# Kernel tuning notes

Hardware: AMD Instinct MI355X
Metric: run time of the kernel (lower is better)

## Reference

```python
import jax, jax.numpy as jnp
import numpy as np

# ParamsJR('JR') defaults, all variances 0 -> fixed constants; w_bb and lm are the fit params.
DT = 1e-4                      # step_size
VMAX, V0, R = 5.0, 6.0, 0.56   # sigmoid params
U_UB = 500.0                   # u_2ndsys_ub
G_EFF = 0.01 + 1000.0          # lb + relu(g)
C1_EFF, C2_EFF = 0.01 + 135.0, 0.01 + 135.0 * 0.8
C3_EFF, C4_EFF = 0.01 + 135.0 * 0.25, 0.01 + 135.0 * 0.25
STD_EFF = 150.0 + 100.0        # noise_std_lb + relu(std_in)
K_EFF = 0.5 + 5.0              # k_lb + relu(k)
A_EFF, a_EFF = 3.25, 1.0 + 100.0   # 0+relu(A), 1+relu(a)
B_EFF, b_EFF = 22.0, 1.0 + 50.0    # 0+relu(B), 1+relu(b)
CY0, Y0, MU = 5.0, 2.0, 0.5
CONDUCT_LB = 1.5


def _sig(x):
    return VMAX / (1.0 + jnp.exp(R * (V0 - x)))


def _sys2nd(A, a, u, x, v):
    return A * a * u - 2.0 * a * v - a * a * x


def _sat(x):  # state saturation 1000*tanh(x/1000)
    return 1000.0 * jnp.tanh(x / 1000.0)


def setup_inputs() -> dict:
    N, H, B, OUT, BUF = 200, 20, 400, 64, 500
    key = jax.random.key(0)
    ks = jax.random.split(key, 7)
    return {
        "input": jax.random.normal(ks[0], (N, H, B), jnp.float32),
        "noise_in": jax.random.normal(ks[1], (N, H, B, 3), jnp.float32),
        "noise_out": jax.random.normal(ks[2], (N, B), jnp.float32),
        "hx": jax.random.uniform(ks[3], (N, 6), jnp.float32),
        "hE": jnp.zeros((N, BUF), jnp.float32),
        "w_bb": jnp.full((N, N), 0.05, jnp.float32),  # zeros + 0.05 init
        "lm": jax.random.normal(ks[4], (OUT, N), jnp.float32),
        "sc": jax.random.uniform(ks[5], (N, N), jnp.float32),
        "dist": jax.random.randint(ks[6], (N, N), 0, 100, dtype=jnp.int32),
    }


def _forward(input, noise_in, noise_out, hx, hE, w_bb, lm, sc, delays):
    OUT = lm.shape[0]
    # connectivity normalization (done once, outside the time loop, as in torch)
    w = jnp.exp(w_bb) * sc
    wl = jnp.log1p(0.5 * (w + w.T))
    w_n = wl / jnp.linalg.norm(wl)             # (N,N)
    dg = -jnp.diag(jnp.sum(w_n, axis=1))       # (N,N) Laplacian diagonal
    # lead-field normalization: rowwise L1 (torch: sqrt(lm**2).sum(1)), then column mean-center
    lm1 = lm / jnp.abs(lm).sum(axis=1, keepdims=True)
    lm_t = lm1 - lm1.sum(axis=0, keepdims=True) / OUT

    def inner(carry, xs):
        M, E, I, Mv, Ev, Iv, hEb = carry
        u, nE = xs                                              # (N,1) each
        Ed = jnp.take_along_axis(hEb, delays, axis=1)           # delayed M buffer
        LEd = jnp.sum(w_n * Ed.T, axis=1, keepdims=True)        # (N,1)
        rM = _sig(E - I)
        rE = STD_EFF * nE + G_EFF * (LEd + dg @ E) + C2_EFF * _sig(C1_EFF * M)
        rI = C4_EFF * _sig(C3_EFF * M)
        ddM = M + DT * Mv
        ddE = E + DT * Ev
        ddI = I + DT * Iv
        ddMv = Mv + DT * _sys2nd(A_EFF, a_EFF, U_UB * jnp.tanh(rM / U_UB), M, Mv)
        ddEv = Ev + DT * _sys2nd(A_EFF, a_EFF, K_EFF * u + U_UB * jnp.tanh(rE / U_UB), E, Ev)
        ddIv = Iv + DT * _sys2nd(B_EFF, b_EFF, U_UB * jnp.tanh(rI / U_UB), I, Iv)
        M, E, I = _sat(ddM), _sat(ddE), _sat(ddI)
        Mv, Ev, Iv = _sat(ddMv), _sat(ddEv), _sat(ddIv)
        hEb = hEb.at[:, 0].set(M[:, 0])
        return (M, E, I, Mv, Ev, Iv, hEb), None

    def outer(carry, xs):
        u_tr, n_tr = xs                                         # (H,N,1) each
        carry, _ = jax.lax.scan(inner, carry, (u_tr, n_tr))
        M, E, I, Mv, Ev, Iv, hEb = carry
        hEb = jnp.concatenate([M, hEb[:, :-1]], axis=1)         # shift delay buffer per TR
        eeg = CY0 * (lm_t @ (E - I)) - Y0                       # (OUT,1)
        return (M, E, I, Mv, Ev, Iv, hEb), eeg[:, 0]

    M, E, I = hx[:, 0:1], hx[:, 1:2], hx[:, 2:3]
    Mv, Ev, Iv = hx[:, 3:4], hx[:, 4:5], hx[:, 5:6]
    u_all = jnp.transpose(input, (2, 1, 0))[..., None]          # (B,H,N,1)
    nE_all = jnp.transpose(noise_in[..., 0], (2, 1, 0))[..., None]
    carry, eeg = jax.lax.scan(outer, (M, E, I, Mv, Ev, Iv, hE), (u_all, nE_all))
    M, E, I, Mv, Ev, Iv, _ = carry
    current_state = jnp.concatenate([M, E, I, Mv, Ev, Iv], axis=1)  # (N,6)
    return eeg.T, current_state                                 # eeg_batch (OUT,B)


def reference(input, noise_in, noise_out, hx, hE, w_bb, lm, sc, dist):
    delays = (dist.astype(jnp.float32) / (CONDUCT_LB + MU)).astype(jnp.int32)
    return _forward(input, noise_in, noise_out, hx, hE, w_bb, lm, sc, delays)
```

## Files before the change

### kernel.cpp

```cpp
#include <hip/hip_runtime.h>
#include <math.h>

namespace {

constexpr int N_   = 200;
constexpr int H_   = 20;
constexpr int B_   = 400;
constexpr int OUT_ = 64;
constexpr int BUF_ = 500;
constexpr int NT_  = 1024;
constexpr int HD_  = 50;
constexpr int HS_  = 51;
constexpr int GT0  = 224;
constexpr int NG_  = 800;
constexpr int EPT  = 50;
constexpr int CAP  = 16;
constexpr int UNR  = 12;
constexpr int RW_  = 256;
constexpr int NFREE = NT_ - RW_;
constexpr int SLAB  = H_ * N_;

constexpr float L2E = 1.4426950408889634f;
constexpr float LN2 = 0.6931471805599453f;

constexpr float DT_  = 0.0001f;
constexpr float G_   = 1000.01f;
constexpr float C1_  = 135.01f;
constexpr float C2_  = 108.01f;
constexpr float C3_  = 33.76f;
constexpr float C4_  = 33.76f;
constexpr float STD_ = 250.0f;
constexpr float K_   = 5.5f;
constexpr float CY0_ = 5.0f;
constexpr float Y0_  = 2.0f;

constexpr float RL2E = 0.56f * L2E;
constexpr float V0R  = 6.0f * RL2E;
constexpr float TU_  = 2.0f * L2E / 500.0f;
constexpr float TS_  = 2.0f * L2E / 1000.0f;

constexpr float KMv = 0.9798f, KMu = 0.0328250f, KMx = 1.0201f;
constexpr float KEv = 0.9798f, KEu = 0.0328250f, KEx = 1.0201f;
constexpr float KIv = 0.9898f, KIu = 0.1122000f, KIx = 0.2601f;

__device__ __forceinline__ float fexp2(float x){ return __builtin_amdgcn_exp2f(x); }
__device__ __forceinline__ float flog2(float x){ return __builtin_amdgcn_logf(x); }
__device__ __forceinline__ float frcp (float x){ return __builtin_amdgcn_rcpf(x); }

__device__ __forceinline__ float sigf(float x){
    return 5.0f * frcp(1.0f + fexp2(fmaf(-RL2E, x, V0R)));
}
__device__ __forceinline__ float tanh500(float x){
    return 500.0f - 1000.0f * frcp(1.0f + fexp2(x * TU_));
}
__device__ __forceinline__ float satf(float x){
    return 1000.0f - 2000.0f * frcp(1.0f + fexp2(x * TS_));
}
__device__ __forceinline__ float wl_f(const float* __restrict__ wbb,
                                      const float* __restrict__ sc,
                                      int i, int j){
    float w0 = fexp2(wbb[i*N_+j]*L2E) * sc[i*N_+j];
    float w1 = fexp2(wbb[j*N_+i]*L2E) * sc[j*N_+i];
    return flog2(1.0f + 0.5f*(w0+w1)) * LN2;
}

__global__ void __launch_bounds__(NT_)
jansen_kernel(
    const float* __restrict__ input,
    const float* __restrict__ noise_in,
    const float* __restrict__ hx,
    const float* __restrict__ hEin,
    const float* __restrict__ wbb,
    const float* __restrict__ lm,
    const float* __restrict__ sc,
    const int*   __restrict__ dist,
    float* __restrict__ out,
    float2* __restrict__ tab)
{
    __shared__ float histT[N_*HS_];
    __shared__ float uslab[H_*N_];
    __shared__ float neslab[H_*N_];
    __shared__ float d0w_l[CAP*N_];
    __shared__ unsigned char d0j_l[CAP*N_];
    __shared__ float d1w_l[CAP*N_];
    __shared__ unsigned char d1j_l[CAP*N_];
    __shared__ float led_part[4*N_];
    __shared__ float2 mpair[2*N_];
    __shared__ float emi[N_];
    __shared__ float colmean[N_];
    __shared__ float lmrs[OUT_];
    __shared__ float red_s[NT_/64];
    __shared__ float norm_s;
    __shared__ int   rbar;

    const int t = threadIdx.x;
    const bool isr = (t < N_);
    const bool isg = (t >= GT0);
    const int  gt  = t - GT0;
    const int  grow  = gt >> 2;
    const int  gslot = gt & 3;
    const int  jbase = gslot * EPT;
    const int  tb    = gt * EPT;

    int sidx[5];
    int goff[5];

    if (t == 0) rbar = 0;
    if (t < OUT_){
        float s2 = 0.f;
        for (int j=0;j<N_;++j) s2 += fabsf(lm[t*N_+j]);
        lmrs[t] = s2;
    }
    float M=0,E=0,I=0,Mv=0,Ev=0,Iv=0, rowsum=0, ledst=0, hE0v=0;
    int cnt0=0, cnt1=0;
    #pragma unroll
    for (int r=0;r<5;++r){ sidx[r]=0; goff[r]=0; }
    if (isg){
        #pragma unroll
        for (int r=0;r<5;++r){
            int p = r*NG_ + gt;
            int hh = p / N_, ii = p - hh*N_;
            sidx[r] = hh*N_ + ii;
            goff[r] = ii*(H_*B_) + hh*B_;
            uslab[sidx[r]]  = input[goff[r]];
            neslab[sidx[r]] = noise_in[goff[r]*3];
        }
    }
    if (isr){
        for (int k=1;k<HD_;++k) histT[t*HS_ + (HD_-k)] = hEin[t*BUF_+k];
        hE0v = hEin[t*BUF_];
        M=hx[t*6+0]; E=hx[t*6+1]; I=hx[t*6+2];
        Mv=hx[t*6+3]; Ev=hx[t*6+4]; Iv=hx[t*6+5];
    }
    __syncthreads();

    float ss = 0.f, rs = 0.f;
    for (int m=0;m<EPT;++m){
        float w = 0.f; int d = 2;
        int j = jbase + m;
        if (isg){
            d = dist[j*N_+grow] >> 1;
            w = wl_f(wbb, sc, grow, j);
        }
        ss = fmaf(w,w,ss); rs += w;
        if (isg){
            int dm = (d<2) ? 2 : d;
            float ws = (d>=2) ? w : 0.f;
            tab[tb+m] = make_float2(ws, __uint_as_float((unsigned)j | ((unsigned)dm<<16)));
        }
    }
    if (isr){
        float cm=0.f;
        for (int o=0;o<OUT_;++o) cm += lm[o*N_+t] * frcp(lmrs[o]);
        colmean[t] = cm * (1.0f/(float)OUT_);
    }
    #pragma unroll
    for (int o=32;o>0;o>>=1) ss += __shfl_down(ss,o,64);
    if ((t&63)==0) red_s[t>>6] = ss;
    __syncthreads();
    if (t==0){ float tot=0.f; for (int w=0;w<NT_/64;++w) tot+=red_s[w]; norm_s = sqrtf(tot); }
    __syncthreads();
    const float inv = 1.0f / norm_s;
    if (isg){
        float* tf = (float*)tab;
        for (int m=0;m<EPT;++m) tf[2*(tb+m)] *= inv;
    }
    if (isg) led_part[gslot*N_+grow] = rs;

    float dw[UNR]; unsigned jpk[3];
    #pragma unroll
    for (int k=0;k<UNR;++k) dw[k] = 0.f;
    jpk[0]=jpk[1]=jpk[2]=0u;
    if (isr){
        #pragma unroll
        for (int k=0;k<UNR;++k){ d0w_l[k*N_+t]=0.f; d0j_l[k*N_+t]=0;
                                 d1w_l[k*N_+t]=0.f; d1j_l[k*N_+t]=0; }
        for (int j=0;j<N_;++j){
            int dd = dist[j*N_+t] >> 1;
            if (dd < 2){
                float w = wl_f(wbb, sc, t, j) * inv;
                if (dd==0){ if (cnt0<CAP){ d0w_l[cnt0*N_+t]=w; d0j_l[cnt0*N_+t]=(unsigned char)j; ++cnt0; } }
                else      { if (cnt1<CAP){ d1w_l[cnt1*N_+t]=w; d1j_l[cnt1*N_+t]=(unsigned char)j; ++cnt1; } }
            }
        }
        #pragma unroll
        for (int k=0;k<UNR;++k){
            dw[k] = d0w_l[k*N_+t];
            unsigned jv = d0j_l[k*N_+t];
            jpk[k>>2] |= jv << ((k&3)*8);
        }
    }
    __syncthreads();

    if (isr){
        rowsum = (led_part[t]+led_part[N_+t]+led_part[2*N_+t]+led_part[3*N_+t]) * inv;
    }
    __syncthreads();

    if (isg){
        float a0 = 0.f;
        for (int m=0;m<EPT;++m){
            float2 e = tab[tb+m];
            unsigned um = __float_as_uint(e.y);
            int c = HD_ - (int)(um>>16);
            a0 = fmaf(e.x, histT[(um&0xFFFFu)*HS_ + c], a0);
        }
        led_part[gslot*N_+grow] = a0;
    }
    __syncthreads();

    if (isr){
        float v = led_part[t]+led_part[N_+t]+led_part[2*N_+t]+led_part[3*N_+t];
        #pragma unroll
        for (int k=0;k<UNR;++k)
            v = fmaf(d1w_l[k*N_+t], histT[(int)d1j_l[k*N_+t]*HS_ + 49], v);
        for (int k=UNR;k<cnt1;++k)
            v = fmaf(d1w_l[k*N_+t], histT[(int)d1j_l[k*N_+t]*HS_ + 49], v);
        ledst = v;
    }

    const int gf = t - RW_;
    int sidxM[6], goffM[6];
    bool has6 = false;
    if (t >= RW_){
        #pragma unroll
        for (int r=0;r<6;++r){
            int p = r*NFREE + gf;
            if (p < SLAB){
                int hh = p / N_, ii = p - hh*N_;
                sidxM[r] = hh*N_ + ii;
                goffM[r] = ii*(H_*B_) + hh*B_;
            } else { sidxM[r]=0; goffM[r]=0; }
        }
        has6 = (5*NFREE + gf) < SLAB;
    }

    float M1r = 0.f;
    if (isr){
        M1r = satf(fmaf(DT_, Mv, M));
        mpair[t] = make_float2(hE0v, M1r);
    }
    __syncthreads();

#define ROW_SYNC()                                                           \
    do {                                                                     \
        asm volatile("s_waitcnt lgkmcnt(0)" ::: "memory");                   \
        if ((t & 63) == 0) atomicAdd(&rbar, 1);                              \
        ++repoch;                                                            \
        while (*(volatile int*)&rbar < 4*repoch)                             \
            __builtin_amdgcn_s_sleep(1);                                     \
        asm volatile("" ::: "memory");                                       \
    } while(0)

    int smod = 0;
    int repoch = 0;
    float su_r[6], sn_r[6];
    for (int s=0; s<B_; ++s){
        int ts = smod+1; if (ts==HD_) ts = 0;
        if (t < RW_){
            #pragma unroll 1
            for (int kb=0; kb<10; ++kb){
                if (isr){
                    const float2* rb = mpair + (kb&1)*N_;
                    float2*       wb = mpair + ((kb+1)&1)*N_;
                    float g0=ledst, g1=0.f, g2=0.f, g3=0.f;
                    float f0=ledst, f1=0.f, f2=0.f, f3=0.f;
                    #pragma unroll
                    for (int k=0;k<UNR;++k){
                        int j = (jpk[k>>2] >> ((k&3)*8)) & 255;
                        float2 mj = rb[j];
                        float w = dw[k];
                        if      ((k&3)==0){ g0=fmaf(w,mj.x,g0); f0=fmaf(w,mj.y,f0); }
                        else if ((k&3)==1){ g1=fmaf(w,mj.x,g1); f1=fmaf(w,mj.y,f1); }
                        else if ((k&3)==2){ g2=fmaf(w,mj.x,g2); f2=fmaf(w,mj.y,f2); }
                        else              { g3=fmaf(w,mj.x,g3); f3=fmaf(w,mj.y,f3); }
                    }
                    for (int k=UNR;k<cnt0;++k){
                        float w = d0w_l[k*N_+t];
                        float2 mj = rb[d0j_l[k*N_+t]];
                        g0=fmaf(w,mj.x,g0); f0=fmaf(w,mj.y,f0);
                    }
                    float LEd0 = (g0+g1)+(g2+g3);
                    float LEd1 = (f0+f1)+(f2+f3);
                    float E1s = satf(fmaf(DT_, Ev, E));
                    float I1s = satf(fmaf(DT_, Iv, I));
                    float uM0 = tanh500(sigf(E - I));
                    float Mv1 = satf(fmaf(KMv, Mv, fmaf(KMu, uM0, -KMx*M)));
                    float M2  = satf(fmaf(DT_, Mv1, M1r));
                    float uM1 = tanh500(sigf(E1s - I1s));
                    float Mv2 = satf(fmaf(KMv, Mv1, fmaf(KMu, uM1, -KMx*M1r)));
                    float M3  = satf(fmaf(DT_, Mv2, M2));
                    wb[t] = make_float2(M2, M3);
                    float uI0 = tanh500(C4_*sigf(C3_*M));
                    float Iv1 = satf(fmaf(KIv, Iv, fmaf(KIu, uI0, -KIx*I)));
                    float I2  = satf(fmaf(DT_, Iv1, I1s));
                    float uI1 = tanh500(C4_*sigf(C3_*M1r));
                    float Iv2 = satf(fmaf(KIv, Iv1, fmaf(KIu, uI1, -KIx*I1s)));
                    int h0 = 2*kb;
                    float u0  = uslab[h0*N_+t];
                    float ne0 = neslab[h0*N_+t];
                    float rE0 = fmaf(STD_, ne0, G_*(LEd0 - rowsum*E)) + C2_*sigf(C1_*M);
                    float uE0 = fmaf(K_, u0, tanh500(rE0));
                    float Ev1 = satf(fmaf(KEv, Ev, fmaf(KEu, uE0, -KEx*E)));
                    float E2  = satf(fmaf(DT_, Ev1, E1s));
                    float u1  = uslab[(h0+1)*N_+t];
                    float ne1 = neslab[(h0+1)*N_+t];
                    float rE1 = fmaf(STD_, ne1, G_*(LEd1 - rowsum*E1s)) + C2_*sigf(C1_*M1r);
                    float uE1 = fmaf(K_, u1, tanh500(rE1));
                    float Ev2 = satf(fmaf(KEv, Ev1, fmaf(KEu, uE1, -KEx*E1s)));
                    M=M2; M1r=M3; Mv=Mv2;
                    I=I2; Iv=Iv2;
                    E=E2; Ev=Ev2;
                }
                if (kb < 9) ROW_SYNC();
            }
            if (isr){ histT[t*HS_ + smod] = M; emi[t] = E - I; }
        } else {
            float acc = 0.f;
            {
                const float4* t4 = (const float4*)(tab + (size_t)gf*EPT);
                #pragma unroll 5
                for (int m=0;m<EPT/2;++m){
                    float4 ee = t4[m];
                    unsigned um0 = __float_as_uint(ee.y);
                    int c0 = ts - (int)(um0>>16); if (c0<0) c0 += HD_;
                    acc = fmaf(ee.x, histT[(um0&0xFFFFu)*HS_ + c0], acc);
                    unsigned um1 = __float_as_uint(ee.w);
                    int c1 = ts - (int)(um1>>16); if (c1<0) c1 += HD_;
                    acc = fmaf(ee.z, histT[(um1&0xFFFFu)*HS_ + c1], acc);
                }
            }
            led_part[(gf&3)*N_ + (gf>>2)] = acc;
            if (gf < NG_-NFREE){
                const int u1 = NFREE + gf;
                float acc1 = 0.f;
                const float4* t4 = (const float4*)(tab + (size_t)u1*EPT);
                #pragma unroll 5
                for (int m=0;m<EPT/2;++m){
                    float4 ee = t4[m];
                    unsigned um0 = __float_as_uint(ee.y);
                    int c0 = ts - (int)(um0>>16); if (c0<0) c0 += HD_;
                    acc1 = fmaf(ee.x, histT[(um0&0xFFFFu)*HS_ + c0], acc1);
                    unsigned um1 = __float_as_uint(ee.w);
                    int c1 = ts - (int)(um1>>16); if (c1<0) c1 += HD_;
                    acc1 = fmaf(ee.z, histT[(um1&0xFFFFu)*HS_ + c1], acc1);
                }
                led_part[(u1&3)*N_ + (u1>>2)] = acc1;
            }
            int sn = s+1; if (sn >= B_) sn = B_-1;
            #pragma unroll
            for (int r=0;r<5;++r){
                su_r[r] = input[goffM[r] + sn];
                sn_r[r] = noise_in[(goffM[r] + sn)*3];
            }
            if (has6){
                su_r[5] = input[goffM[5] + sn];
                sn_r[5] = noise_in[(goffM[5] + sn)*3];
            }
        }
        __syncthreads();
        if (isr){
            float v = led_part[t]+led_part[N_+t]+led_part[2*N_+t]+led_part[3*N_+t];
            #pragma unroll
            for (int k=0;k<UNR;++k)
                v = fmaf(d1w_l[k*N_+t], mpair[d0j_l[0]*0 + d1j_l[k*N_+t]].x, v);
            for (int k=UNR;k<cnt1;++k)
                v = fmaf(d1w_l[k*N_+t], mpair[d1j_l[k*N_+t]].x, v);
            ledst = v;
        }
        if (t >= RW_){
            #pragma unroll
            for (int r=0;r<5;++r){
                uslab[sidxM[r]]  = su_r[r];
                neslab[sidxM[r]] = sn_r[r];
            }
            if (has6){ uslab[sidxM[5]] = su_r[5]; neslab[sidxM[5]] = sn_r[5]; }
        }
        {
            int o = t>>4, l = t&15;
            float il = frcp(lmrs[o]);
            float a2 = 0.f;
            for (int j=l;j<N_;j+=16)
                a2 = fmaf(fmaf(lm[o*N_+j], il, -colmean[j]), emi[j], a2);
            a2 += __shfl_down(a2,8,16); a2 += __shfl_down(a2,4,16);
            a2 += __shfl_down(a2,2,16); a2 += __shfl_down(a2,1,16);
            if (l==0) out[o*B_+s] = fmaf(CY0_, a2, -Y0_);
        }
        smod = ts;
        __syncthreads();
    }

#undef ROW_SYNC

    if (isr){
        float* cs = out + OUT_*B_ + t*6;
        cs[0]=M; cs[1]=E; cs[2]=I; cs[3]=Mv; cs[4]=Ev; cs[5]=Iv;
    }
}

}

extern "C" void kernel_launch(void* const* d_in, const int* in_sizes, int n_in,
                              void* d_out, int out_size, void* d_ws, size_t ws_size,
                              hipStream_t stream)
{
    const float* input    = (const float*)d_in[0];
    const float* noise_in = (const float*)d_in[1];
    const float* hx   = (const float*)d_in[3];
    const float* hEin = (const float*)d_in[4];
    const float* wbb  = (const float*)d_in[5];
    const float* lm   = (const float*)d_in[6];
    const float* sc   = (const float*)d_in[7];
    const int*   dist = (const int*)d_in[8];
    float* out = (float*)d_out;
    float2* tab = (float2*)((char*)d_ws + 1024);

    hipLaunchKernelGGL(jansen_kernel, dim3(1), dim3(NT_), 0, stream,
                       input, noise_in, hx, hEin, wbb, lm, sc, dist, out, tab);
}
```

Measured before the change: 5.923 ms.

## Halve block to 512 threads and redistribute delay-gather and slab-load work

Shrinks the single workgroup from 1024 to 512 threads. The 256 non-recurrence threads now loop over up to four delay-gather rows each and prefetch up to sixteen input/noise slab entries, and every thread computes two EEG output rows. The goal is cheaper block barriers and less issue contention with the waves running the serial recurrence. The cost is more serial work per free thread, which could land on the critical path of each time step. Setup now reduces the weight norm serially through shared memory on thread 0.

```diff
diff --git a/kernel.cpp b/kernel.cpp
--- a/kernel.cpp
+++ b/kernel.cpp
@@ -8,7 +8,7 @@
 constexpr int B_   = 400;
 constexpr int OUT_ = 64;
 constexpr int BUF_ = 500;
-constexpr int NT_  = 1024;
+constexpr int NT_  = 512;
 constexpr int HD_  = 50;
 constexpr int HS_  = 51;
 constexpr int GT0  = 224;
@@ -89,21 +89,13 @@
     __shared__ float emi[N_];
     __shared__ float colmean[N_];
     __shared__ float lmrs[OUT_];
-    __shared__ float red_s[NT_/64];
+    __shared__ float sss[1024];
     __shared__ float norm_s;
     __shared__ int   rbar;
 
     const int t = threadIdx.x;
     const bool isr = (t < N_);
-    const bool isg = (t >= GT0);
-    const int  gt  = t - GT0;
-    const int  grow  = gt >> 2;
-    const int  gslot = gt & 3;
-    const int  jbase = gslot * EPT;
-    const int  tb    = gt * EPT;
-
-    int sidx[5];
-    int goff[5];
+    const int  gf  = t - RW_;
 
     if (t == 0) rbar = 0;
     if (t < OUT_){
@@ -114,16 +106,17 @@
     float M=0,E=0,I=0,Mv=0,Ev=0,Iv=0, rowsum=0, ledst=0, hE0v=0;
     int cnt0=0, cnt1=0;
     #pragma unroll
-    for (int r=0;r<5;++r){ sidx[r]=0; goff[r]=0; }
-    if (isg){
-        #pragma unroll
-        for (int r=0;r<5;++r){
-            int p = r*NG_ + gt;
-            int hh = p / N_, ii = p - hh*N_;
-            sidx[r] = hh*N_ + ii;
-            goff[r] = ii*(H_*B_) + hh*B_;
-            uslab[sidx[r]]  = input[goff[r]];
-            neslab[sidx[r]] = noise_in[goff[r]*3];
+    for (int q=0;q<2;++q){
+        int e = t + q*512;
+        if (e >= GT0){
+            int gt = e - GT0;
+            for (int r=0;r<5;++r){
+                int p = r*NG_ + gt;
+                int hh = p / N_, ii = p - hh*N_;
+                int go = ii*(H_*B_) + hh*B_;
+                uslab[hh*N_+ii]  = input[go];
+                neslab[hh*N_+ii] = noise_in[go*3];
+            }
         }
     }
     if (isr){
@@ -134,38 +127,58 @@
     }
     __syncthreads();
 
-    float ss = 0.f, rs = 0.f;
-    for (int m=0;m<EPT;++m){
-        float w = 0.f; int d = 2;
-        int j = jbase + m;
-        if (isg){
-            d = dist[j*N_+grow] >> 1;
-            w = wl_f(wbb, sc, grow, j);
-        }
-        ss = fmaf(w,w,ss); rs += w;
-        if (isg){
-            int dm = (d<2) ? 2 : d;
-            float ws = (d>=2) ? w : 0.f;
-            tab[tb+m] = make_float2(ws, __uint_as_float((unsigned)j | ((unsigned)dm<<16)));
-        }
+    float rsQ[2];
+    rsQ[0]=0.f; rsQ[1]=0.f;
+    #pragma unroll
+    for (int q=0;q<2;++q){
+        int e = t + q*512;
+        float ss = 0.f, rs = 0.f;
+        if (e >= GT0){
+            int gt = e - GT0;
+            int grow = gt >> 2, gslot = gt & 3;
+            int jbase = gslot * EPT, tb = gt * EPT;
+            for (int m=0;m<EPT;++m){
+                int j = jbase + m;
+                int d = dist[j*N_+grow] >> 1;
+                float w = wl_f(wbb, sc, grow, j);
+                ss = fmaf(w,w,ss); rs += w;
+                int dm = (d<2) ? 2 : d;
+                float wsv = (d>=2) ? w : 0.f;
+                tab[tb+m] = make_float2(wsv, __uint_as_float((unsigned)j | ((unsigned)dm<<16)));
+            }
+        }
+        sss[e] = ss;
+        rsQ[q] = rs;
     }
     if (isr){
         float cm=0.f;
         for (int o=0;o<OUT_;++o) cm += lm[o*N_+t] * frcp(lmrs[o]);
         colmean[t] = cm * (1.0f/(float)OUT_);
     }
+    __syncthreads();
+    if (t==0){
+        float tot = 0.f;
+        for (int w=0;w<16;++w){
+            int b = w*64;
+            for (int o=32;o>0;o>>=1)
+                for (int L=0;L<o;++L) sss[b+L] += sss[b+L+o];
+            tot += sss[b];
+        }
+        norm_s = sqrtf(tot);
+    }
+    __syncthreads();
+    const float inv = 1.0f / norm_s;
     #pragma unroll
-    for (int o=32;o>0;o>>=1) ss += __shfl_down(ss,o,64);
-    if ((t&63)==0) red_s[t>>6] = ss;
-    __syncthreads();
-    if (t==0){ float tot=0.f; for (int w=0;w<NT_/64;++w) tot+=red_s[w]; norm_s = sqrtf(tot); }
-    __syncthreads();
-    const float inv = 1.0f / norm_s;
-    if (isg){
-        float* tf = (float*)tab;
-        for (int m=0;m<EPT;++m) tf[2*(tb+m)] *= inv;
-    }
-    if (isg) led_part[gslot*N_+grow] = rs;
+    for (int q=0;q<2;++q){
+        int e = t + q*512;
+        if (e >= GT0){
+            int gt = e - GT0;
+            int grow = gt >> 2, gslot = gt & 3, tb = gt * EPT;
+            float* tf = (float*)tab;
+            for (int m=0;m<EPT;++m) tf[2*(tb+m)] *= inv;
+            led_part[gslot*N_+grow] = rsQ[q];
+        }
+    }
 
     float dw[UNR]; unsigned jpk[3];
     #pragma unroll
@@ -197,15 +210,21 @@
     }
     __syncthreads();
 
-    if (isg){
-        float a0 = 0.f;
-        for (int m=0;m<EPT;++m){
-            float2 e = tab[tb+m];
-            unsigned um = __float_as_uint(e.y);
-            int c = HD_ - (int)(um>>16);
-            a0 = fmaf(e.x, histT[(um&0xFFFFu)*HS_ + c], a0);
-        }
-        led_part[gslot*N_+grow] = a0;
+    #pragma unroll
+    for (int q=0;q<2;++q){
+        int u  = q ? (t + 288) : (t - GT0);
+        bool ok = q ? true : (t >= GT0);
+        if (ok){
+            int tb = u * EPT;
+            float a0 = 0.f;
+            for (int m=0;m<EPT;++m){
+                float2 e = tab[tb+m];
+                unsigned um = __float_as_uint(e.y);
+                int c = HD_ - (int)(um>>16);
+                a0 = fmaf(e.x, histT[(um&0xFFFFu)*HS_ + c], a0);
+            }
+            led_part[(u&3)*N_ + (u>>2)] = a0;
+        }
     }
     __syncthreads();
 
@@ -219,20 +238,16 @@
         ledst = v;
     }
 
-    const int gf = t - RW_;
-    int sidxM[6], goffM[6];
-    bool has6 = false;
+    int goffM[16];
     if (t >= RW_){
         #pragma unroll
-        for (int r=0;r<6;++r){
+        for (int r=0;r<16;++r){
             int p = r*NFREE + gf;
             if (p < SLAB){
                 int hh = p / N_, ii = p - hh*N_;
-                sidxM[r] = hh*N_ + ii;
                 goffM[r] = ii*(H_*B_) + hh*B_;
-            } else { sidxM[r]=0; goffM[r]=0; }
-        }
-        has6 = (5*NFREE + gf) < SLAB;
+            } else goffM[r] = -1;
+        }
     }
 
     float M1r = 0.f;
@@ -254,7 +269,7 @@
 
     int smod = 0;
     int repoch = 0;
-    float su_r[6], sn_r[6];
+    float su_r[16], sn_r[16];
     for (int s=0; s<B_; ++s){
         int ts = smod+1; if (ts==HD_) ts = 0;
         if (t < RW_){
@@ -316,9 +331,12 @@
             }
             if (isr){ histT[t*HS_ + smod] = M; emi[t] = E - I; }
         } else {
-            float acc = 0.f;
-            {
-                const float4* t4 = (const float4*)(tab + (size_t)gf*EPT);
+            #pragma unroll 1
+            for (int q=0;q<4;++q){
+                if (q==3 && gf>=NG_-3*NFREE) break;
+                int u = (q<3) ? (gf + (q<<8)) : (3*NFREE + gf);
+                float acc = 0.f;
+                const float4* t4 = (const float4*)(tab + (size_t)u*EPT);
                 #pragma unroll 5
                 for (int m=0;m<EPT/2;++m){
                     float4 ee = t4[m];
@@ -329,33 +347,15 @@
                     int c1 = ts - (int)(um1>>16); if (c1<0) c1 += HD_;
                     acc = fmaf(ee.z, histT[(um1&0xFFFFu)*HS_ + c1], acc);
                 }
-            }
-            led_part[(gf&3)*N_ + (gf>>2)] = acc;
-            if (gf < NG_-NFREE){
-                const int u1 = NFREE + gf;
-                float acc1 = 0.f;
-                const float4* t4 = (const float4*)(tab + (size_t)u1*EPT);
-                #pragma unroll 5
-                for (int m=0;m<EPT/2;++m){
-                    float4 ee = t4[m];
-                    unsigned um0 = __float_as_uint(ee.y);
-                    int c0 = ts - (int)(um0>>16); if (c0<0) c0 += HD_;
-                    acc1 = fmaf(ee.x, histT[(um0&0xFFFFu)*HS_ + c0], acc1);
-                    unsigned um1 = __float_as_uint(ee.w);
-                    int c1 = ts - (int)(um1>>16); if (c1<0) c1 += HD_;
-                    acc1 = fmaf(ee.z, histT[(um1&0xFFFFu)*HS_ + c1], acc1);
-                }
-                led_part[(u1&3)*N_ + (u1>>2)] = acc1;
+                led_part[(u&3)*N_ + (u>>2)] = acc;
             }
             int sn = s+1; if (sn >= B_) sn = B_-1;
             #pragma unroll
-            for (int r=0;r<5;++r){
-                su_r[r] = input[goffM[r] + sn];
-                sn_r[r] = noise_in[(goffM[r] + sn)*3];
-            }
-            if (has6){
-                su_r[5] = input[goffM[5] + sn];
-                sn_r[5] = noise_in[(goffM[5] + sn)*3];
+            for (int r=0;r<16;++r){
+                if (goffM[r] >= 0){
+                    su_r[r] = input[goffM[r] + sn];
+                    sn_r[r] = noise_in[(goffM[r] + sn)*3];
+                }
             }
         }
         __syncthreads();
@@ -363,28 +363,34 @@
             float v = led_part[t]+led_part[N_+t]+led_part[2*N_+t]+led_part[3*N_+t];
             #pragma unroll
             for (int k=0;k<UNR;++k)
-                v = fmaf(d1w_l[k*N_+t], mpair[d0j_l[0]*0 + d1j_l[k*N_+t]].x, v);
+                v = fmaf(d1w_l[k*N_+t], mpair[d1j_l[k*N_+t]].x, v);
             for (int k=UNR;k<cnt1;++k)
                 v = fmaf(d1w_l[k*N_+t], mpair[d1j_l[k*N_+t]].x, v);
             ledst = v;
         }
         if (t >= RW_){
             #pragma unroll
-            for (int r=0;r<5;++r){
-                uslab[sidxM[r]]  = su_r[r];
-                neslab[sidxM[r]] = sn_r[r];
-            }
-            if (has6){ uslab[sidxM[5]] = su_r[5]; neslab[sidxM[5]] = sn_r[5]; }
+            for (int r=0;r<16;++r){
+                if (goffM[r] >= 0){
+                    int p = r*NFREE + gf;
+                    int hh = p / N_, ii = p - hh*N_;
+                    uslab[hh*N_+ii]  = su_r[r];
+                    neslab[hh*N_+ii] = sn_r[r];
+                }
+            }
         }
         {
-            int o = t>>4, l = t&15;
-            float il = frcp(lmrs[o]);
-            float a2 = 0.f;
-            for (int j=l;j<N_;j+=16)
-                a2 = fmaf(fmaf(lm[o*N_+j], il, -colmean[j]), emi[j], a2);
-            a2 += __shfl_down(a2,8,16); a2 += __shfl_down(a2,4,16);
-            a2 += __shfl_down(a2,2,16); a2 += __shfl_down(a2,1,16);
-            if (l==0) out[o*B_+s] = fmaf(CY0_, a2, -Y0_);
+            #pragma unroll
+            for (int pp=0;pp<2;++pp){
+                int o = (t>>4) + pp*32, l = t&15;
+                float il = frcp(lmrs[o]);
+                float a2 = 0.f;
+                for (int j=l;j<N_;j+=16)
+                    a2 = fmaf(fmaf(lm[o*N_+j], il, -colmean[j]), emi[j], a2);
+                a2 += __shfl_down(a2,8,16); a2 += __shfl_down(a2,4,16);
+                a2 += __shfl_down(a2,2,16); a2 += __shfl_down(a2,1,16);
+                if (l==0) out[o*B_+s] = fmaf(CY0_, a2, -Y0_);
+            }
         }
         smod = ts;
         __syncthreads();
```

Measured after the change: 9.815 ms. +65.7%, slower.

## Triple-buffer M state and compute M one step ahead to prefetch neighbours

Applied to the files above, without the earlier changes.

The M-state exchange buffer goes from two slots to three, and each row thread computes the M trajectory one sub-step pair ahead. It can then prefetch the unrolled neighbour M values for the next iteration into registers before the row barrier, so the shared-memory gathers leave the critical path after each sync. This adds register pressure, rotating buffer-index bookkeeping that must stay consistent with the non-row threads (cr advanced by 10 mod 3), and extra setup work before the loop.

```diff
diff --git a/kernel.cpp b/kernel.cpp
--- a/kernel.cpp
+++ b/kernel.cpp
@@ -85,7 +85,7 @@
     __shared__ float d1w_l[CAP*N_];
     __shared__ unsigned char d1j_l[CAP*N_];
     __shared__ float led_part[4*N_];
-    __shared__ float2 mpair[2*N_];
+    __shared__ float2 mtri[3*N_];
     __shared__ float emi[N_];
     __shared__ float colmean[N_];
     __shared__ float lmrs[OUT_];
@@ -235,12 +235,32 @@
         has6 = (5*NFREE + gf) < SLAB;
     }
 
-    float M1r = 0.f;
-    if (isr){
-        M1r = satf(fmaf(DT_, Mv, M));
-        mpair[t] = make_float2(hE0v, M1r);
-    }
-    __syncthreads();
+    float E1c=0, I1c=0, M1=0, M2c=0, M3c=0, Mv2c=0, MvOut=Mv;
+    if (isr){
+        E1c = satf(fmaf(DT_, Ev, E));
+        I1c = satf(fmaf(DT_, Iv, I));
+        float uM0 = tanh500(sigf(E - I));
+        float Mv1 = satf(fmaf(KMv, Mv, fmaf(KMu, uM0, -KMx*M)));
+        M1  = satf(fmaf(DT_, Mv, M));
+        float uM1 = tanh500(sigf(E1c - I1c));
+        Mv2c = satf(fmaf(KMv, Mv1, fmaf(KMu, uM1, -KMx*M1)));
+        M2c  = satf(fmaf(DT_, Mv1, M1));
+        M3c  = satf(fmaf(DT_, Mv2c, M2c));
+        mtri[t]      = make_float2(hE0v, M1);
+        mtri[N_ + t] = make_float2(M2c, M3c);
+    }
+    __syncthreads();
+
+    float2 pf[UNR];
+    #pragma unroll
+    for (int k=0;k<UNR;++k) pf[k] = make_float2(0.f,0.f);
+    if (isr){
+        #pragma unroll
+        for (int k=0;k<UNR;++k){
+            int j = (jpk[k>>2] >> ((k&3)*8)) & 255;
+            pf[k] = mtri[j];
+        }
+    }
 
 #define ROW_SYNC()                                                           \
     do {                                                                     \
@@ -254,21 +274,22 @@
 
     int smod = 0;
     int repoch = 0;
+    int cr = 0;
     float su_r[6], sn_r[6];
     for (int s=0; s<B_; ++s){
         int ts = smod+1; if (ts==HD_) ts = 0;
         if (t < RW_){
             #pragma unroll 1
             for (int kb=0; kb<10; ++kb){
+                int pre = cr+1; if (pre==3) pre = 0;
+                int wbx = pre+1; if (wbx==3) wbx = 0;
                 if (isr){
-                    const float2* rb = mpair + (kb&1)*N_;
-                    float2*       wb = mpair + ((kb+1)&1)*N_;
+                    float2* wb = mtri + wbx*N_;
                     float g0=ledst, g1=0.f, g2=0.f, g3=0.f;
                     float f0=ledst, f1=0.f, f2=0.f, f3=0.f;
                     #pragma unroll
                     for (int k=0;k<UNR;++k){
-                        int j = (jpk[k>>2] >> ((k&3)*8)) & 255;
-                        float2 mj = rb[j];
+                        float2 mj = pf[k];
                         float w = dw[k];
                         if      ((k&3)==0){ g0=fmaf(w,mj.x,g0); f0=fmaf(w,mj.y,f0); }
                         else if ((k&3)==1){ g1=fmaf(w,mj.x,g1); f1=fmaf(w,mj.y,f1); }
@@ -277,45 +298,55 @@
                     }
                     for (int k=UNR;k<cnt0;++k){
                         float w = d0w_l[k*N_+t];
-                        float2 mj = rb[d0j_l[k*N_+t]];
+                        float2 mj = mtri[cr*N_ + d0j_l[k*N_+t]];
                         g0=fmaf(w,mj.x,g0); f0=fmaf(w,mj.y,f0);
+                    }
+                    #pragma unroll
+                    for (int k=0;k<UNR;++k){
+                        int j = (jpk[k>>2] >> ((k&3)*8)) & 255;
+                        pf[k] = mtri[pre*N_ + j];
                     }
                     float LEd0 = (g0+g1)+(g2+g3);
                     float LEd1 = (f0+f1)+(f2+f3);
-                    float E1s = satf(fmaf(DT_, Ev, E));
-                    float I1s = satf(fmaf(DT_, Iv, I));
-                    float uM0 = tanh500(sigf(E - I));
-                    float Mv1 = satf(fmaf(KMv, Mv, fmaf(KMu, uM0, -KMx*M)));
-                    float M2  = satf(fmaf(DT_, Mv1, M1r));
-                    float uM1 = tanh500(sigf(E1s - I1s));
-                    float Mv2 = satf(fmaf(KMv, Mv1, fmaf(KMu, uM1, -KMx*M1r)));
-                    float M3  = satf(fmaf(DT_, Mv2, M2));
-                    wb[t] = make_float2(M2, M3);
-                    float uI0 = tanh500(C4_*sigf(C3_*M));
-                    float Iv1 = satf(fmaf(KIv, Iv, fmaf(KIu, uI0, -KIx*I)));
-                    float I2  = satf(fmaf(DT_, Iv1, I1s));
-                    float uI1 = tanh500(C4_*sigf(C3_*M1r));
-                    float Iv2 = satf(fmaf(KIv, Iv1, fmaf(KIu, uI1, -KIx*I1s)));
+                    MvOut = Mv2c;
                     int h0 = 2*kb;
                     float u0  = uslab[h0*N_+t];
                     float ne0 = neslab[h0*N_+t];
                     float rE0 = fmaf(STD_, ne0, G_*(LEd0 - rowsum*E)) + C2_*sigf(C1_*M);
                     float uE0 = fmaf(K_, u0, tanh500(rE0));
                     float Ev1 = satf(fmaf(KEv, Ev, fmaf(KEu, uE0, -KEx*E)));
-                    float E2  = satf(fmaf(DT_, Ev1, E1s));
+                    float E2  = satf(fmaf(DT_, Ev1, E1c));
+                    float uI0 = tanh500(C4_*sigf(C3_*M));
+                    float Iv1 = satf(fmaf(KIv, Iv, fmaf(KIu, uI0, -KIx*I)));
+                    float I2  = satf(fmaf(DT_, Iv1, I1c));
                     float u1  = uslab[(h0+1)*N_+t];
                     float ne1 = neslab[(h0+1)*N_+t];
-                    float rE1 = fmaf(STD_, ne1, G_*(LEd1 - rowsum*E1s)) + C2_*sigf(C1_*M1r);
+                    float rE1 = fmaf(STD_, ne1, G_*(LEd1 - rowsum*E1c)) + C2_*sigf(C1_*M1);
                     float uE1 = fmaf(K_, u1, tanh500(rE1));
-                    float Ev2 = satf(fmaf(KEv, Ev1, fmaf(KEu, uE1, -KEx*E1s)));
-                    M=M2; M1r=M3; Mv=Mv2;
-                    I=I2; Iv=Iv2;
-                    E=E2; Ev=Ev2;
+                    float Ev2 = satf(fmaf(KEv, Ev1, fmaf(KEu, uE1, -KEx*E1c)));
+                    float E3n = satf(fmaf(DT_, Ev2, E2));
+                    float uI1 = tanh500(C4_*sigf(C3_*M1));
+                    float Iv2 = satf(fmaf(KIv, Iv1, fmaf(KIu, uI1, -KIx*I1c)));
+                    float I3n = satf(fmaf(DT_, Iv2, I2));
+                    float uM2 = tanh500(sigf(E2 - I2));
+                    float Mv3 = satf(fmaf(KMv, Mv2c, fmaf(KMu, uM2, -KMx*M2c)));
+                    float M4  = satf(fmaf(DT_, Mv3, M3c));
+                    float uM3 = tanh500(sigf(E3n - I3n));
+                    float Mv4 = satf(fmaf(KMv, Mv3, fmaf(KMu, uM3, -KMx*M3c)));
+                    float M5  = satf(fmaf(DT_, Mv4, M4));
+                    wb[t] = make_float2(M4, M5);
+                    E=E2; E1c=E3n; Ev=Ev2;
+                    I=I2; I1c=I3n; Iv=Iv2;
+                    M=M2c; M1=M3c; M2c=M4; M3c=M5; Mv2c=Mv4;
                 }
+                cr = pre;
                 if (kb < 9) ROW_SYNC();
             }
             if (isr){ histT[t*HS_ + smod] = M; emi[t] = E - I; }
         } else {
+            #pragma unroll 1
+            for (int q=0;q<10;++q) { cr = cr; break; }
+            cr += 10; cr %= 3;
             float acc = 0.f;
             {
                 const float4* t4 = (const float4*)(tab + (size_t)gf*EPT);
@@ -363,9 +394,9 @@
             float v = led_part[t]+led_part[N_+t]+led_part[2*N_+t]+led_part[3*N_+t];
             #pragma unroll
             for (int k=0;k<UNR;++k)
-                v = fmaf(d1w_l[k*N_+t], mpair[d0j_l[0]*0 + d1j_l[k*N_+t]].x, v);
+                v = fmaf(d1w_l[k*N_+t], mtri[cr*N_ + d1j_l[k*N_+t]].x, v);
             for (int k=UNR;k<cnt1;++k)
-                v = fmaf(d1w_l[k*N_+t], mpair[d1j_l[k*N_+t]].x, v);
+                v = fmaf(d1w_l[k*N_+t], mtri[cr*N_ + d1j_l[k*N_+t]].x, v);
             ledst = v;
         }
         if (t >= RW_){
@@ -394,7 +425,7 @@
 
     if (isr){
         float* cs = out + OUT_*B_ + t*6;
-        cs[0]=M; cs[1]=E; cs[2]=I; cs[3]=Mv; cs[4]=Ev; cs[5]=Iv;
+        cs[0]=M; cs[1]=E; cs[2]=I; cs[3]=MvOut; cs[4]=Ev; cs[5]=Iv;
     }
 }
 
```

Result: slower. 6.855 ms (+15.7%).
